# Kernel optimization log

Hardware: AMD Instinct MI355X
Metric: run time of the kernel (lower is better)

## Reference

```python
import jax, jax.numpy as jnp
import numpy as np

NC_MEM = 64          # nTemporalMemoryChannels
NC_IMG = 64          # nImageFeatureChannels
FTL_RATIO = 0.5      # temporalFTLRatio
N_BLOCKS = 3         # nTemporalBlocks
B, H, W = 32, 64, 96
M = 32               # memory buffer length (= max(memory_idx)+1)


def setup_inputs() -> dict:
    key = jax.random.key(0)
    ks = jax.random.split(key, 8)
    eye = jnp.eye(4, dtype=jnp.float32)
    img_features = jax.random.normal(ks[0], (B, NC_IMG, H, W), jnp.float32)
    prev_mem_features = jax.random.normal(ks[1], (M, NC_MEM, H, W), jnp.float32)
    # extrinsics: random perturbation around identity so torch.inverse-equivalent is well conditioned
    prev_extrinsics = 0.1 * jax.random.normal(ks[2], (M, 4, 4), jnp.float32) + eye
    cur_extrinsics = 0.1 * jax.random.normal(ks[3], (B, 4, 4), jnp.float32) + eye
    memory_idx = jnp.arange(B, dtype=jnp.int32)
    use_memory = jax.random.randint(ks[4], (B,), 0, 2).astype(bool)
    NC = NC_MEM + NC_IMG
    Ws = jax.random.normal(ks[5], (N_BLOCKS, NC, NC), jnp.float32) * (1.0 / np.sqrt(NC))
    bs = jax.random.normal(ks[6], (N_BLOCKS, NC), jnp.float32) * 0.01
    return {
        "img_features": img_features,
        "prev_mem_features": prev_mem_features,
        "prev_extrinsics": prev_extrinsics,
        "cur_extrinsics": cur_extrinsics,
        "memory_idx": memory_idx,
        "use_memory": use_memory,
        "Ws": Ws,
        "bs": bs,
    }


def _apply_ftl(xf, feats, ratio):
    # Feature Transform Layer: first `ratio` fraction of channels (rounded down
    # to a multiple of 4) treated as groups of homogeneous 4-vectors per pixel,
    # warped by the 4x4 transform xf; remaining channels pass through.
    b, c, h, w = feats.shape
    nc_ftl = (int(c * ratio) // 4) * 4
    g = nc_ftl // 4
    pts = feats[:, :nc_ftl].reshape(b, g, 4, h * w)
    pts = jnp.einsum("bij,bgjp->bgip", xf, pts).reshape(b, nc_ftl, h, w)
    return jnp.concatenate([pts, feats[:, nc_ftl:]], axis=1)


def reference(img_features, prev_mem_features, prev_extrinsics, cur_extrinsics,
              memory_idx, use_memory, Ws, bs):
    eye = jnp.eye(4, dtype=prev_extrinsics.dtype)
    # --- transform_memory_features (gather + extrinsics warp, masked) ---
    mem_g = prev_mem_features[memory_idx]              # [B, NC_MEM, H, W]
    prev_ext_g = prev_extrinsics[memory_idx]           # [B, 4, 4]
    # entries with use_memory=False are zeroed; guard inverse with identity
    safe_prev = jnp.where(use_memory[:, None, None], prev_ext_g, eye)
    prev_cam0_to_world = jnp.linalg.inv(safe_prev)
    xf = jnp.einsum("bij,bjk->bik", cur_extrinsics, prev_cam0_to_world)
    mem_xfed = _apply_ftl(xf, mem_g, FTL_RATIO)
    mem_xfed = jnp.where(use_memory[:, None, None, None], mem_xfed,
                         jnp.zeros((), mem_xfed.dtype))
    # --- forward_one_step: concat + 1x1 conv stack (pointwise matmuls) ---
    x = jnp.concatenate([mem_xfed, img_features], axis=1)  # [B, 128, H, W]
    n = Ws.shape[0]
    for i in range(n):
        x = jnp.einsum("oc,bchw->bohw", Ws[i], x) + bs[i][None, :, None, None]
        if i != n - 1:
            x = jax.nn.relu(x)
    fused_features = x[:, NC_MEM:]                     # returned output
    return fused_features
```

## Files before the change

### kernel.cpp

```cpp
#include <hip/hip_runtime.h>
#include <hip/hip_fp16.h>

#define NC_MEM 64
#define NC_IMG 64
#define NC     128
#define B_     32
#define H_     64
#define W_     96
#define HW_    (H_ * W_)
#define P_TILE 128
#define NTILES (HW_ / P_TILE)
#define FS     520
#define FOFF(pt, ks) ((((pt) * 4) + (ks)) * FS)
#define XOFF(pt, ks, blk) (FOFF(pt, ks) + ((((blk) + (pt)) & 63) << 3))

#define WA_HI  0
#define WA_LO  98304
#define XF_OFF 196608
#define UM_OFF 198656

typedef _Float16 f16x8 __attribute__((ext_vector_type(8)));
typedef __attribute__((ext_vector_type(4))) float f32x4;

__device__ inline unsigned pk2h(float a, float b) {
    __half2 h = __floats2half2_rn(a, b);
    return *(const unsigned*)&h;
}

__global__ void prep(const float* __restrict__ Ws,
                     const float* __restrict__ prev_ext,
                     const float* __restrict__ cur_ext,
                     const int* __restrict__ mem_idx,
                     const unsigned char* __restrict__ um_raw,
                     unsigned char* __restrict__ wsb) {
    if (blockIdx.x < 192) {
        int idx = blockIdx.x * 256 + threadIdx.x;
        int l = idx >> 14, r = idx & 16383, o = r >> 7, c = r & 127;
        float w = Ws[idx];
        __half hi = __float2half_rn(w);
        __half lo = __float2half_rn(w - __half2float(hi));
        int mt = o >> 4, lm = o & 15, ks = c >> 5, kr = c & 31, q = kr >> 3, j = kr & 7;
        int lane = q * 16 + lm;
        int di = ((((l * 8 + mt) * 4 + ks) * 64 + lane) << 3) + j;
        ((unsigned short*)(wsb + WA_HI))[di] = __half_as_ushort(hi);
        ((unsigned short*)(wsb + WA_LO))[di] = __half_as_ushort(lo);
        return;
    }
    int tb = threadIdx.x;
    if (tb >= 64) return;
    bool flag = (tb < 32) && (tb & 3) && (um_raw[tb] != 0);
    bool is_bool = __any(flag);
    if (tb >= B_) return;
    int b = tb;
    bool um = is_bool ? (um_raw[b] != 0) : (((const int*)um_raw)[b] != 0);
    int mi = mem_idx[b];

    float a[16];
#pragma unroll
    for (int i = 0; i < 16; ++i)
        a[i] = um ? prev_ext[mi * 16 + i] : ((i % 5 == 0) ? 1.f : 0.f);

    float s0 = a[0]*a[5]  - a[1]*a[4];
    float s1 = a[0]*a[6]  - a[2]*a[4];
    float s2 = a[0]*a[7]  - a[3]*a[4];
    float s3 = a[1]*a[6]  - a[2]*a[5];
    float s4 = a[1]*a[7]  - a[3]*a[5];
    float s5 = a[2]*a[7]  - a[3]*a[6];
    float c5 = a[10]*a[15] - a[11]*a[14];
    float c4 = a[9]*a[15]  - a[11]*a[13];
    float c3 = a[9]*a[14]  - a[10]*a[13];
    float c2 = a[8]*a[15]  - a[11]*a[12];
    float c1 = a[8]*a[14]  - a[10]*a[12];
    float c0 = a[8]*a[13]  - a[9]*a[12];
    float det = s0*c5 - s1*c4 + s2*c3 + s3*c2 - s4*c1 + s5*c0;
    float id = 1.0f / det;

    float inv[16];
    inv[0]  = ( a[5]*c5  - a[6]*c4  + a[7]*c3)  * id;
    inv[1]  = (-a[1]*c5  + a[2]*c4  - a[3]*c3)  * id;
    inv[2]  = ( a[13]*s5 - a[14]*s4 + a[15]*s3) * id;
    inv[3]  = (-a[9]*s5  + a[10]*s4 - a[11]*s3) * id;
    inv[4]  = (-a[4]*c5  + a[6]*c2  - a[7]*c1)  * id;
    inv[5]  = ( a[0]*c5  - a[2]*c2  + a[3]*c1)  * id;
    inv[6]  = (-a[12]*s5 + a[14]*s2 - a[15]*s1) * id;
    inv[7]  = ( a[8]*s5  - a[10]*s2 + a[11]*s1) * id;
    inv[8]  = ( a[4]*c4  - a[5]*c2  + a[7]*c0)  * id;
    inv[9]  = (-a[0]*c4  + a[1]*c2  - a[3]*c0)  * id;
    inv[10] = ( a[12]*s4 - a[13]*s2 + a[15]*s0) * id;
    inv[11] = (-a[8]*s4  + a[9]*s2  - a[11]*s0) * id;
    inv[12] = (-a[4]*c3  + a[5]*c1  - a[6]*c0)  * id;
    inv[13] = ( a[0]*c3  - a[1]*c1  + a[2]*c0)  * id;
    inv[14] = (-a[12]*s3 + a[13]*s1 - a[14]*s0) * id;
    inv[15] = ( a[8]*s3  - a[9]*s1  + a[10]*s0) * id;

    float* xf = (float*)(wsb + XF_OFF) + b * 16;
#pragma unroll
    for (int i = 0; i < 4; ++i)
#pragma unroll
        for (int j2 = 0; j2 < 4; ++j2) {
            float s = 0.f;
#pragma unroll
            for (int k = 0; k < 4; ++k)
                s += cur_ext[b * 16 + i * 4 + k] * inv[k * 4 + j2];
            xf[i * 4 + j2] = s;
        }
    ((float*)(wsb + UM_OFF))[b] = um ? 1.f : 0.f;
}

__global__ __launch_bounds__(512, 4)
void fused_main(const float* __restrict__ img, const float* __restrict__ mem,
                const int* __restrict__ mem_idx, const float* __restrict__ bs,
                const unsigned char* __restrict__ wsb, float* __restrict__ out) {
    __shared__ unsigned short xh[32 * FS];

    const int t   = threadIdx.x;
    const int b   = blockIdx.y;
    const int hw0 = blockIdx.x * P_TILE;
    const bool umb = ((const float*)(wsb + UM_OFF))[b] != 0.f;
    const int mi  = mem_idx[b];

    const f16x8* __restrict__ WH = (const f16x8*)(wsb + WA_HI);
    const f16x8* __restrict__ WL = (const f16x8*)(wsb + WA_LO);

    const int w    = t >> 6;
    const int lane = t & 63;
    const int wq   = lane >> 4;
    const int lm   = lane & 15;
    const int mt0  = 2 * (w & 3);
    const int nt0  = 4 * (w >> 2);

#define FI(l, mt, ks) (((((l) * 8 + (mt)) * 4) + (ks)) * 64 + lane)

    {
        const int q   = ((t & 7) << 2) | ((t >> 3) & 3);
        const int og  = t >> 5;
        const int px0 = hw0 + q * 4;
        const int pt  = q >> 2;
        if (umb) {
            const int c0 = og * 8;
            const float* basep = (c0 < NC_MEM)
                ? (mem + ((size_t)mi * NC_MEM + c0) * HW_ + px0)
                : (img + ((size_t)b * NC_IMG + (c0 - NC_MEM)) * HW_ + px0);
            f32x4 v[8];
#pragma unroll
            for (int cc = 0; cc < 8; ++cc)
                v[cc] = *(const f32x4*)(basep + (size_t)cc * HW_);
            if (og < 4) {
                float xfv[16];
                const float* xfp = (const float*)(wsb + XF_OFF) + b * 16;
#pragma unroll
                for (int j = 0; j < 4; ++j)
                    *(f32x4*)&xfv[j * 4] = *(const f32x4*)&xfp[j * 4];
#pragma unroll
                for (int sg = 0; sg < 2; ++sg) {
#pragma unroll
                    for (int i = 0; i < 4; ++i) {
                        float a0 = v[4*sg+0][i], a1 = v[4*sg+1][i];
                        float a2 = v[4*sg+2][i], a3 = v[4*sg+3][i];
                        v[4*sg+0][i] = xfv[0]*a0  + xfv[1]*a1  + xfv[2]*a2  + xfv[3]*a3;
                        v[4*sg+1][i] = xfv[4]*a0  + xfv[5]*a1  + xfv[6]*a2  + xfv[7]*a3;
                        v[4*sg+2][i] = xfv[8]*a0  + xfv[9]*a1  + xfv[10]*a2 + xfv[11]*a3;
                        v[4*sg+3][i] = xfv[12]*a0 + xfv[13]*a1 + xfv[14]*a2 + xfv[15]*a3;
                    }
                }
            }
            const int bk0 = (og & 3) * 16 + (q & 3) * 4;
#pragma unroll
            for (int i = 0; i < 4; ++i) {
                uint4 pk;
                pk.x = pk2h(v[0][i], v[1][i]);
                pk.y = pk2h(v[2][i], v[3][i]);
                pk.z = pk2h(v[4][i], v[5][i]);
                pk.w = pk2h(v[6][i], v[7][i]);
                *(uint4*)&xh[XOFF(pt, og >> 2, bk0 + i)] = pk;
            }
        } else {
            const int gg = 16 + og;
            const int c0 = gg * 4 - NC_MEM;
            f32x4 u[4];
#pragma unroll
            for (int cc = 0; cc < 4; ++cc)
                u[cc] = *(const f32x4*)(img + ((size_t)b * NC_IMG + c0 + cc) * HW_ + px0);
            const int bk0 = ((gg & 7) >> 1) * 16 + (q & 3) * 4;
            const int hoff = (gg & 1) * 4;
#pragma unroll
            for (int i = 0; i < 4; ++i)
                *(uint2*)&xh[XOFF(pt, gg >> 3, bk0 + i) + hoff] =
                    make_uint2(pk2h(u[0][i], u[1][i]), pk2h(u[2][i], u[3][i]));
        }
    }

    const int kpa = umb ? 0 : 2, kpb = umb ? 1 : 3;
    f16x8 p0h = WH[FI(0, mt0,     kpa)], p0l = WL[FI(0, mt0,     kpa)];
    f16x8 p1h = WH[FI(0, mt0 + 1, kpa)], p1l = WL[FI(0, mt0 + 1, kpa)];
    f16x8 p2h = WH[FI(0, mt0,     kpb)], p2l = WL[FI(0, mt0,     kpb)];
    f16x8 p3h = WH[FI(0, mt0 + 1, kpb)], p3l = WL[FI(0, mt0 + 1, kpb)];

    __syncthreads();

    f32x4 acc[2][4];

    auto run_ks = [&](int ks, f16x8 ah0, f16x8 al0, f16x8 ah1, f16x8 al1) {
#pragma unroll
        for (int nt = 0; nt < 4; ++nt) {
            f16x8 bh = *(const f16x8*)&xh[XOFF(nt0 + nt, ks, lane)];
            acc[0][nt] = __builtin_amdgcn_mfma_f32_16x16x32_f16(ah0, bh, acc[0][nt], 0, 0, 0);
            acc[1][nt] = __builtin_amdgcn_mfma_f32_16x16x32_f16(ah1, bh, acc[1][nt], 0, 0, 0);
            acc[0][nt] = __builtin_amdgcn_mfma_f32_16x16x32_f16(al0, bh, acc[0][nt], 0, 0, 0);
            acc[1][nt] = __builtin_amdgcn_mfma_f32_16x16x32_f16(al1, bh, acc[1][nt], 0, 0, 0);
        }
    };
    auto writeback = [&]() {
#pragma unroll
        for (int mi2 = 0; mi2 < 2; ++mi2) {
            const int mt = mt0 + mi2;
            const int ks2 = mt >> 1;
            const int lane_f = ((mt & 1) * 2 + (wq >> 1)) * 16 + lm;
            const int j0 = (wq & 1) * 4;
#pragma unroll
            for (int nt = 0; nt < 4; ++nt) {
                float v0 = fmaxf(acc[mi2][nt][0], 0.f);
                float v1 = fmaxf(acc[mi2][nt][1], 0.f);
                float v2 = fmaxf(acc[mi2][nt][2], 0.f);
                float v3 = fmaxf(acc[mi2][nt][3], 0.f);
                *(uint2*)&xh[XOFF(nt0 + nt, ks2, lane_f) + j0] =
                    make_uint2(pk2h(v0, v1), pk2h(v2, v3));
            }
        }
    };

#pragma unroll
    for (int mi2 = 0; mi2 < 2; ++mi2) {
        f32x4 bv = *(const f32x4*)&bs[0 * NC + (mt0 + mi2) * 16 + wq * 4];
#pragma unroll
        for (int nt = 0; nt < 4; ++nt) acc[mi2][nt] = bv;
    }
    __builtin_amdgcn_s_setprio(1);
    if (umb) {
        run_ks(0, p0h, p0l, p1h, p1l);
        run_ks(1, p2h, p2l, p3h, p3l);
        run_ks(2, WH[FI(0, mt0, 2)], WL[FI(0, mt0, 2)],
                  WH[FI(0, mt0 + 1, 2)], WL[FI(0, mt0 + 1, 2)]);
        run_ks(3, WH[FI(0, mt0, 3)], WL[FI(0, mt0, 3)],
                  WH[FI(0, mt0 + 1, 3)], WL[FI(0, mt0 + 1, 3)]);
    } else {
        run_ks(2, p0h, p0l, p1h, p1l);
        run_ks(3, p2h, p2l, p3h, p3l);
    }
    __builtin_amdgcn_s_setprio(0);
    f16x8 q0h = WH[FI(1, mt0, 0)],     q0l = WL[FI(1, mt0, 0)];
    f16x8 q1h = WH[FI(1, mt0 + 1, 0)], q1l = WL[FI(1, mt0 + 1, 0)];
    f16x8 q2h = WH[FI(1, mt0, 1)],     q2l = WL[FI(1, mt0, 1)];
    f16x8 q3h = WH[FI(1, mt0 + 1, 1)], q3l = WL[FI(1, mt0 + 1, 1)];
    __syncthreads();
    writeback();
    __syncthreads();

#pragma unroll
    for (int mi2 = 0; mi2 < 2; ++mi2) {
        f32x4 bv = *(const f32x4*)&bs[1 * NC + (mt0 + mi2) * 16 + wq * 4];
#pragma unroll
        for (int nt = 0; nt < 4; ++nt) acc[mi2][nt] = bv;
    }
    __builtin_amdgcn_s_setprio(1);
    run_ks(0, q0h, q0l, q1h, q1l);
    run_ks(1, q2h, q2l, q3h, q3l);
    run_ks(2, WH[FI(1, mt0, 2)], WL[FI(1, mt0, 2)],
              WH[FI(1, mt0 + 1, 2)], WL[FI(1, mt0 + 1, 2)]);
    run_ks(3, WH[FI(1, mt0, 3)], WL[FI(1, mt0, 3)],
              WH[FI(1, mt0 + 1, 3)], WL[FI(1, mt0 + 1, 3)]);
    __builtin_amdgcn_s_setprio(0);
    const int mt2 = 4 + (w & 3);
    f16x8 r0h = WH[FI(2, mt2, 0)], r0l = WL[FI(2, mt2, 0)];
    f16x8 r1h = WH[FI(2, mt2, 1)], r1l = WL[FI(2, mt2, 1)];
    f16x8 r2h = WH[FI(2, mt2, 2)], r2l = WL[FI(2, mt2, 2)];
    f16x8 r3h = WH[FI(2, mt2, 3)], r3l = WL[FI(2, mt2, 3)];
    __syncthreads();
    writeback();
    __syncthreads();

    {
        f32x4 a2[4];
        f32x4 bv = *(const f32x4*)&bs[2 * NC + mt2 * 16 + wq * 4];
#pragma unroll
        for (int nt = 0; nt < 4; ++nt) a2[nt] = bv;
        auto run2 = [&](int ks, f16x8 ah, f16x8 al) {
#pragma unroll
            for (int nt = 0; nt < 4; ++nt) {
                f16x8 bh = *(const f16x8*)&xh[XOFF(nt0 + nt, ks, lane)];
                a2[nt] = __builtin_amdgcn_mfma_f32_16x16x32_f16(ah, bh, a2[nt], 0, 0, 0);
                a2[nt] = __builtin_amdgcn_mfma_f32_16x16x32_f16(al, bh, a2[nt], 0, 0, 0);
            }
        };
        __builtin_amdgcn_s_setprio(1);
        run2(0, r0h, r0l);
        run2(1, r1h, r1l);
        run2(2, r2h, r2l);
        run2(3, r3h, r3l);
        __builtin_amdgcn_s_setprio(0);
        const int oc0 = mt2 * 16 + wq * 4 - 64;
#pragma unroll
        for (int nt = 0; nt < 4; ++nt) {
            float* dst = out + ((size_t)b * 64 + oc0) * HW_ + hw0 + (nt0 + nt) * 16 + lm;
#pragma unroll
            for (int r = 0; r < 4; ++r)
                __builtin_nontemporal_store(a2[nt][r], dst + (size_t)r * HW_);
        }
    }
#undef FI
}

extern "C" void kernel_launch(void* const* d_in, const int* in_sizes, int n_in,
                              void* d_out, int out_size, void* d_ws, size_t ws_size,
                              hipStream_t stream) {
    const float* img  = (const float*)d_in[0];
    const float* mem  = (const float*)d_in[1];
    const float* pext = (const float*)d_in[2];
    const float* cext = (const float*)d_in[3];
    const int*   midx = (const int*)d_in[4];
    const unsigned char* umem = (const unsigned char*)d_in[5];
    const float* Ws   = (const float*)d_in[6];
    const float* bs   = (const float*)d_in[7];
    float* out = (float*)d_out;
    unsigned char* wsb = (unsigned char*)d_ws;

    hipLaunchKernelGGL(prep, dim3(193), dim3(256), 0, stream,
                       Ws, pext, cext, midx, umem, wsb);
    hipLaunchKernelGGL(fused_main, dim3(NTILES, B_), dim3(512), 0, stream,
                       img, mem, midx, bs, wsb, out);
}
```

Baseline: 162.5 us.

## Process two pixel tiles per block with double-buffered LDS and prefetched loads

```diff
diff --git a/kernel.cpp b/kernel.cpp
--- a/kernel.cpp
+++ b/kernel.cpp
@@ -10,6 +10,7 @@
 #define HW_    (H_ * W_)
 #define P_TILE 128
 #define NTILES (HW_ / P_TILE)
+#define T_BLK  2
 #define FS     520
 #define FOFF(pt, ks) ((((pt) * 4) + (ks)) * FS)
 #define XOFF(pt, ks, blk) (FOFF(pt, ks) + ((((blk) + (pt)) & 63) << 3))
@@ -25,6 +26,14 @@
 __device__ inline unsigned pk2h(float a, float b) {
     __half2 h = __floats2half2_rn(a, b);
     return *(const unsigned*)&h;
+}
+
+__device__ inline void bar_lds() {
+    __builtin_amdgcn_sched_barrier(0);
+    asm volatile("s_waitcnt lgkmcnt(0)" ::: "memory");
+    __builtin_amdgcn_s_barrier();
+    asm volatile("" ::: "memory");
+    __builtin_amdgcn_sched_barrier(0);
 }
 
 __global__ void prep(const float* __restrict__ Ws,
@@ -111,13 +120,13 @@
 void fused_main(const float* __restrict__ img, const float* __restrict__ mem,
                 const int* __restrict__ mem_idx, const float* __restrict__ bs,
                 const unsigned char* __restrict__ wsb, float* __restrict__ out) {
-    __shared__ unsigned short xh[32 * FS];
-
-    const int t   = threadIdx.x;
-    const int b   = blockIdx.y;
-    const int hw0 = blockIdx.x * P_TILE;
+    __shared__ unsigned short xh[2][32 * FS];
+
+    const int t    = threadIdx.x;
+    const int b    = blockIdx.y;
+    const int hw00 = blockIdx.x * (P_TILE * T_BLK);
     const bool umb = ((const float*)(wsb + UM_OFF))[b] != 0.f;
-    const int mi  = mem_idx[b];
+    const int mi   = mem_idx[b];
 
     const f16x8* __restrict__ WH = (const f16x8*)(wsb + WA_HI);
     const f16x8* __restrict__ WL = (const f16x8*)(wsb + WA_LO);
@@ -128,23 +137,32 @@
     const int lm   = lane & 15;
     const int mt0  = 2 * (w & 3);
     const int nt0  = 4 * (w >> 2);
-
-#define FI(l, mt, ks) (((((l) * 8 + (mt)) * 4) + (ks)) * 64 + lane)
-
-    {
-        const int q   = ((t & 7) << 2) | ((t >> 3) & 3);
-        const int og  = t >> 5;
-        const int px0 = hw0 + q * 4;
-        const int pt  = q >> 2;
+    const int mt2  = 4 + (w & 3);
+
+    const int q   = ((t & 7) << 2) | ((t >> 3) & 3);
+    const int og  = t >> 5;
+    const int pt  = q >> 2;
+
+    auto stage_load = [&](int hw0t, f32x4* v) {
+        const int px0 = hw0t + q * 4;
         if (umb) {
             const int c0 = og * 8;
             const float* basep = (c0 < NC_MEM)
                 ? (mem + ((size_t)mi * NC_MEM + c0) * HW_ + px0)
                 : (img + ((size_t)b * NC_IMG + (c0 - NC_MEM)) * HW_ + px0);
-            f32x4 v[8];
 #pragma unroll
             for (int cc = 0; cc < 8; ++cc)
                 v[cc] = *(const f32x4*)(basep + (size_t)cc * HW_);
+        } else {
+            const int c0 = og * 4;
+#pragma unroll
+            for (int cc = 0; cc < 4; ++cc)
+                v[cc] = *(const f32x4*)(img + ((size_t)b * NC_IMG + c0 + cc) * HW_ + px0);
+        }
+    };
+
+    auto stage_write = [&](unsigned short* xb, f32x4* v) {
+        if (umb) {
             if (og < 4) {
                 float xfv[16];
                 const float* xfp = (const float*)(wsb + XF_OFF) + b * 16;
@@ -172,45 +190,38 @@
                 pk.y = pk2h(v[2][i], v[3][i]);
                 pk.z = pk2h(v[4][i], v[5][i]);
                 pk.w = pk2h(v[6][i], v[7][i]);
-                *(uint4*)&xh[XOFF(pt, og >> 2, bk0 + i)] = pk;
+                *(uint4*)&xb[XOFF(pt, og >> 2, bk0 + i)] = pk;
             }
         } else {
             const int gg = 16 + og;
-            const int c0 = gg * 4 - NC_MEM;
-            f32x4 u[4];
-#pragma unroll
-            for (int cc = 0; cc < 4; ++cc)
-                u[cc] = *(const f32x4*)(img + ((size_t)b * NC_IMG + c0 + cc) * HW_ + px0);
             const int bk0 = ((gg & 7) >> 1) * 16 + (q & 3) * 4;
             const int hoff = (gg & 1) * 4;
 #pragma unroll
             for (int i = 0; i < 4; ++i)
-                *(uint2*)&xh[XOFF(pt, gg >> 3, bk0 + i) + hoff] =
-                    make_uint2(pk2h(u[0][i], u[1][i]), pk2h(u[2][i], u[3][i]));
-        }
-    }
-
-    const int kpa = umb ? 0 : 2, kpb = umb ? 1 : 3;
-    f16x8 p0h = WH[FI(0, mt0,     kpa)], p0l = WL[FI(0, mt0,     kpa)];
-    f16x8 p1h = WH[FI(0, mt0 + 1, kpa)], p1l = WL[FI(0, mt0 + 1, kpa)];
-    f16x8 p2h = WH[FI(0, mt0,     kpb)], p2l = WL[FI(0, mt0,     kpb)];
-    f16x8 p3h = WH[FI(0, mt0 + 1, kpb)], p3l = WL[FI(0, mt0 + 1, kpb)];
-
-    __syncthreads();
-
-    f32x4 acc[2][4];
-
-    auto run_ks = [&](int ks, f16x8 ah0, f16x8 al0, f16x8 ah1, f16x8 al1) {
+                *(uint2*)&xb[XOFF(pt, gg >> 3, bk0 + i) + hoff] =
+                    make_uint2(pk2h(v[0][i], v[1][i]), pk2h(v[2][i], v[3][i]));
+        }
+    };
+
+    auto run_ks_f = [&](const unsigned short* xc, int ks,
+                        f16x8 ah0, f16x8 al0, f16x8 ah1, f16x8 al1,
+                        f32x4 (&ac)[2][4]) {
 #pragma unroll
         for (int nt = 0; nt < 4; ++nt) {
-            f16x8 bh = *(const f16x8*)&xh[XOFF(nt0 + nt, ks, lane)];
-            acc[0][nt] = __builtin_amdgcn_mfma_f32_16x16x32_f16(ah0, bh, acc[0][nt], 0, 0, 0);
-            acc[1][nt] = __builtin_amdgcn_mfma_f32_16x16x32_f16(ah1, bh, acc[1][nt], 0, 0, 0);
-            acc[0][nt] = __builtin_amdgcn_mfma_f32_16x16x32_f16(al0, bh, acc[0][nt], 0, 0, 0);
-            acc[1][nt] = __builtin_amdgcn_mfma_f32_16x16x32_f16(al1, bh, acc[1][nt], 0, 0, 0);
-        }
-    };
-    auto writeback = [&]() {
+            f16x8 bh = *(const f16x8*)&xc[XOFF(nt0 + nt, ks, lane)];
+            ac[0][nt] = __builtin_amdgcn_mfma_f32_16x16x32_f16(ah0, bh, ac[0][nt], 0, 0, 0);
+            ac[1][nt] = __builtin_amdgcn_mfma_f32_16x16x32_f16(ah1, bh, ac[1][nt], 0, 0, 0);
+            ac[0][nt] = __builtin_amdgcn_mfma_f32_16x16x32_f16(al0, bh, ac[0][nt], 0, 0, 0);
+            ac[1][nt] = __builtin_amdgcn_mfma_f32_16x16x32_f16(al1, bh, ac[1][nt], 0, 0, 0);
+        }
+    };
+    auto run_ks = [&](const unsigned short* xc, const f16x8* WHt, const f16x8* WLt,
+                      int l, int ks, f32x4 (&ac)[2][4]) {
+        int f0 = ((l * 8 + mt0) * 4 + ks) * 64 + lane;
+        int f1 = f0 + 256;
+        run_ks_f(xc, ks, WHt[f0], WLt[f0], WHt[f1], WLt[f1], ac);
+    };
+    auto writeback = [&](unsigned short* xb, f32x4 (&ac)[2][4]) {
 #pragma unroll
         for (int mi2 = 0; mi2 < 2; ++mi2) {
             const int mt = mt0 + mi2;
@@ -219,95 +230,117 @@
             const int j0 = (wq & 1) * 4;
 #pragma unroll
             for (int nt = 0; nt < 4; ++nt) {
-                float v0 = fmaxf(acc[mi2][nt][0], 0.f);
-                float v1 = fmaxf(acc[mi2][nt][1], 0.f);
-                float v2 = fmaxf(acc[mi2][nt][2], 0.f);
-                float v3 = fmaxf(acc[mi2][nt][3], 0.f);
-                *(uint2*)&xh[XOFF(nt0 + nt, ks2, lane_f) + j0] =
+                float v0 = fmaxf(ac[mi2][nt][0], 0.f);
+                float v1 = fmaxf(ac[mi2][nt][1], 0.f);
+                float v2 = fmaxf(ac[mi2][nt][2], 0.f);
+                float v3 = fmaxf(ac[mi2][nt][3], 0.f);
+                *(uint2*)&xb[XOFF(nt0 + nt, ks2, lane_f) + j0] =
                     make_uint2(pk2h(v0, v1), pk2h(v2, v3));
             }
         }
     };
 
-#pragma unroll
-    for (int mi2 = 0; mi2 < 2; ++mi2) {
-        f32x4 bv = *(const f32x4*)&bs[0 * NC + (mt0 + mi2) * 16 + wq * 4];
-#pragma unroll
-        for (int nt = 0; nt < 4; ++nt) acc[mi2][nt] = bv;
+    const int kpa = umb ? 0 : 2, kpb = umb ? 1 : 3;
+    {
+        f32x4 v0[8];
+        stage_load(hw00, v0);
+        stage_write(xh[0], v0);
     }
-    __builtin_amdgcn_s_setprio(1);
-    if (umb) {
-        run_ks(0, p0h, p0l, p1h, p1l);
-        run_ks(1, p2h, p2l, p3h, p3l);
-        run_ks(2, WH[FI(0, mt0, 2)], WL[FI(0, mt0, 2)],
-                  WH[FI(0, mt0 + 1, 2)], WL[FI(0, mt0 + 1, 2)]);
-        run_ks(3, WH[FI(0, mt0, 3)], WL[FI(0, mt0, 3)],
-                  WH[FI(0, mt0 + 1, 3)], WL[FI(0, mt0 + 1, 3)]);
-    } else {
-        run_ks(2, p0h, p0l, p1h, p1l);
-        run_ks(3, p2h, p2l, p3h, p3l);
+    f16x8 pa_h, pa_l, pb_h, pb_l, pc_h, pc_l, pd_h, pd_l;
+    {
+        int f0 = (mt0 * 4 + kpa) * 64 + lane, f1 = f0 + 256;
+        pa_h = WH[f0]; pa_l = WL[f0]; pb_h = WH[f1]; pb_l = WL[f1];
+        int g0 = (mt0 * 4 + kpb) * 64 + lane, g1 = g0 + 256;
+        pc_h = WH[g0]; pc_l = WL[g0]; pd_h = WH[g1]; pd_l = WL[g1];
     }
-    __builtin_amdgcn_s_setprio(0);
-    f16x8 q0h = WH[FI(1, mt0, 0)],     q0l = WL[FI(1, mt0, 0)];
-    f16x8 q1h = WH[FI(1, mt0 + 1, 0)], q1l = WL[FI(1, mt0 + 1, 0)];
-    f16x8 q2h = WH[FI(1, mt0, 1)],     q2l = WL[FI(1, mt0, 1)];
-    f16x8 q3h = WH[FI(1, mt0 + 1, 1)], q3l = WL[FI(1, mt0 + 1, 1)];
-    __syncthreads();
-    writeback();
-    __syncthreads();
-
-#pragma unroll
-    for (int mi2 = 0; mi2 < 2; ++mi2) {
-        f32x4 bv = *(const f32x4*)&bs[1 * NC + (mt0 + mi2) * 16 + wq * 4];
-#pragma unroll
-        for (int nt = 0; nt < 4; ++nt) acc[mi2][nt] = bv;
+    bar_lds();
+
+#pragma unroll
+    for (int tt = 0; tt < T_BLK; ++tt) {
+        unsigned short* xc = xh[tt];
+        unsigned short* xn = xh[tt ^ 1];
+        const int hw0t = hw00 + tt * P_TILE;
+
+        unsigned zo = 0;
+        asm volatile("" : "+s"(zo));
+        const f16x8* WHt = WH + zo;
+        const f16x8* WLt = WL + zo;
+        const float* bst = bs + zo;
+
+        f32x4 vn[8];
+        if (tt + 1 < T_BLK) stage_load(hw0t + P_TILE, vn);
+
+        f32x4 acc[2][4];
+#pragma unroll
+        for (int mi2 = 0; mi2 < 2; ++mi2) {
+            f32x4 bv = *(const f32x4*)&bst[0 * NC + (mt0 + mi2) * 16 + wq * 4];
+#pragma unroll
+            for (int nt = 0; nt < 4; ++nt) acc[mi2][nt] = bv;
+        }
+        __builtin_amdgcn_s_setprio(1);
+        run_ks_f(xc, kpa, pa_h, pa_l, pb_h, pb_l, acc);
+        run_ks_f(xc, kpb, pc_h, pc_l, pd_h, pd_l, acc);
+        if (umb) {
+            run_ks(xc, WHt, WLt, 0, 2, acc);
+            run_ks(xc, WHt, WLt, 0, 3, acc);
+        }
+        __builtin_amdgcn_s_setprio(0);
+        bar_lds();
+        writeback(xc, acc);
+        bar_lds();
+
+#pragma unroll
+        for (int mi2 = 0; mi2 < 2; ++mi2) {
+            f32x4 bv = *(const f32x4*)&bst[1 * NC + (mt0 + mi2) * 16 + wq * 4];
+#pragma unroll
+            for (int nt = 0; nt < 4; ++nt) acc[mi2][nt] = bv;
+        }
+        __builtin_amdgcn_s_setprio(1);
+        run_ks(xc, WHt, WLt, 1, 0, acc);
+        run_ks(xc, WHt, WLt, 1, 1, acc);
+        run_ks(xc, WHt, WLt, 1, 2, acc);
+        run_ks(xc, WHt, WLt, 1, 3, acc);
+        __builtin_amdgcn_s_setprio(0);
+        if (tt + 1 < T_BLK) stage_write(xn, vn);
+        bar_lds();
+        writeback(xc, acc);
+        bar_lds();
+
+        {
+            f32x4 a2[4];
+            f32x4 bv = *(const f32x4*)&bst[2 * NC + mt2 * 16 + wq * 4];
+#pragma unroll
+            for (int nt = 0; nt < 4; ++nt) a2[nt] = bv;
+            __builtin_amdgcn_s_setprio(1);
+#pragma unroll
+            for (int ks = 0; ks < 4; ++ks) {
+                int f = ((2 * 8 + mt2) * 4 + ks) * 64 + lane;
+                f16x8 ah = WHt[f], al = WLt[f];
+#pragma unroll
+                for (int nt = 0; nt < 4; ++nt) {
+                    f16x8 bh = *(const f16x8*)&xc[XOFF(nt0 + nt, ks, lane)];
+                    a2[nt] = __builtin_amdgcn_mfma_f32_16x16x32_f16(ah, bh, a2[nt], 0, 0, 0);
+                    a2[nt] = __builtin_amdgcn_mfma_f32_16x16x32_f16(al, bh, a2[nt], 0, 0, 0);
+                }
+            }
+            __builtin_amdgcn_s_setprio(0);
+            const int oc0 = mt2 * 16 + wq * 4 - 64;
+#pragma unroll
+            for (int nt = 0; nt < 4; ++nt) {
+                float* dst = out + ((size_t)b * 64 + oc0) * HW_ + hw0t + (nt0 + nt) * 16 + lm;
+#pragma unroll
+                for (int r = 0; r < 4; ++r)
+                    __builtin_nontemporal_store(a2[nt][r], dst + (size_t)r * HW_);
+            }
+        }
+        if (tt + 1 < T_BLK) {
+            int f0 = (mt0 * 4 + kpa) * 64 + lane, f1 = f0 + 256;
+            pa_h = WHt[f0]; pa_l = WLt[f0]; pb_h = WHt[f1]; pb_l = WLt[f1];
+            int g0 = (mt0 * 4 + kpb) * 64 + lane, g1 = g0 + 256;
+            pc_h = WHt[g0]; pc_l = WLt[g0]; pd_h = WHt[g1]; pd_l = WLt[g1];
+            bar_lds();
+        }
     }
-    __builtin_amdgcn_s_setprio(1);
-    run_ks(0, q0h, q0l, q1h, q1l);
-    run_ks(1, q2h, q2l, q3h, q3l);
-    run_ks(2, WH[FI(1, mt0, 2)], WL[FI(1, mt0, 2)],
-              WH[FI(1, mt0 + 1, 2)], WL[FI(1, mt0 + 1, 2)]);
-    run_ks(3, WH[FI(1, mt0, 3)], WL[FI(1, mt0, 3)],
-              WH[FI(1, mt0 + 1, 3)], WL[FI(1, mt0 + 1, 3)]);
-    __builtin_amdgcn_s_setprio(0);
-    const int mt2 = 4 + (w & 3);
-    f16x8 r0h = WH[FI(2, mt2, 0)], r0l = WL[FI(2, mt2, 0)];
-    f16x8 r1h = WH[FI(2, mt2, 1)], r1l = WL[FI(2, mt2, 1)];
-    f16x8 r2h = WH[FI(2, mt2, 2)], r2l = WL[FI(2, mt2, 2)];
-    f16x8 r3h = WH[FI(2, mt2, 3)], r3l = WL[FI(2, mt2, 3)];
-    __syncthreads();
-    writeback();
-    __syncthreads();
-
-    {
-        f32x4 a2[4];
-        f32x4 bv = *(const f32x4*)&bs[2 * NC + mt2 * 16 + wq * 4];
-#pragma unroll
-        for (int nt = 0; nt < 4; ++nt) a2[nt] = bv;
-        auto run2 = [&](int ks, f16x8 ah, f16x8 al) {
-#pragma unroll
-            for (int nt = 0; nt < 4; ++nt) {
-                f16x8 bh = *(const f16x8*)&xh[XOFF(nt0 + nt, ks, lane)];
-                a2[nt] = __builtin_amdgcn_mfma_f32_16x16x32_f16(ah, bh, a2[nt], 0, 0, 0);
-                a2[nt] = __builtin_amdgcn_mfma_f32_16x16x32_f16(al, bh, a2[nt], 0, 0, 0);
-            }
-        };
-        __builtin_amdgcn_s_setprio(1);
-        run2(0, r0h, r0l);
-        run2(1, r1h, r1l);
-        run2(2, r2h, r2l);
-        run2(3, r3h, r3l);
-        __builtin_amdgcn_s_setprio(0);
-        const int oc0 = mt2 * 16 + wq * 4 - 64;
-#pragma unroll
-        for (int nt = 0; nt < 4; ++nt) {
-            float* dst = out + ((size_t)b * 64 + oc0) * HW_ + hw0 + (nt0 + nt) * 16 + lm;
-#pragma unroll
-            for (int r = 0; r < 4; ++r)
-                __builtin_nontemporal_store(a2[nt][r], dst + (size_t)r * HW_);
-        }
-    }
-#undef FI
 }
 
 extern "C" void kernel_launch(void* const* d_in, const int* in_sizes, int n_in,
@@ -326,6 +359,6 @@
 
     hipLaunchKernelGGL(prep, dim3(193), dim3(256), 0, stream,
                        Ws, pext, cext, midx, umem, wsb);
-    hipLaunchKernelGGL(fused_main, dim3(NTILES, B_), dim3(512), 0, stream,
+    hipLaunchKernelGGL(fused_main, dim3(NTILES / T_BLK, B_), dim3(512), 0, stream,
                        img, mem, midx, bs, wsb, out);
 }
```

After: 201.5 us. 24.0% more time.
